# Performance work log

Measured on AMD Instinct MI355X. Metric: run time of the kernel, lower is better.

The kernel has to match this reference:

```python
import jax, jax.numpy as jnp
import numpy as np

B, NQ, NP, C, H = 8, 1024, 2048, 1024, 16
D = C // H  # head_dim = 64


def setup_inputs() -> dict:
    key = jax.random.key(0)
    ks = jax.random.split(key, 12)
    s = 1.0 / np.sqrt(C)
    inp = {
        "x": jax.random.normal(ks[0], (B, NQ, C), dtype=jnp.float32),
        "ctx": jax.random.normal(ks[1], (B, NP, C), dtype=jnp.float32),
        "freqs_cis": jax.random.normal(ks[2], (NP, D // 2, 2), dtype=jnp.float32),
        "wq": jax.random.normal(ks[3], (C, C), dtype=jnp.float32) * s,
        "bq": jnp.zeros((C,), dtype=jnp.float32),
        "wk": jax.random.normal(ks[4], (C, C), dtype=jnp.float32) * s,
        "bk": jnp.zeros((C,), dtype=jnp.float32),
        "wv": jax.random.normal(ks[5], (C, C), dtype=jnp.float32) * s,
        "bv": jnp.zeros((C,), dtype=jnp.float32),
        "wo": jax.random.normal(ks[6], (C, C), dtype=jnp.float32) * s,
        "bo": jnp.zeros((C,), dtype=jnp.float32),
    }
    return inp


def _apply_rope(k, freqs_cis):
    # k: [B, Np, H, D]; freqs_cis: [Np, D//2, 2] (cos, sin)
    b, n, h, d = k.shape
    kp = k.reshape(b, n, h, d // 2, 2)  # adjacent-pair complex convention
    kr, ki = kp[..., 0], kp[..., 1]
    cos = freqs_cis[None, :, None, :, 0]
    sin = freqs_cis[None, :, None, :, 1]
    out_r = kr * cos - ki * sin
    out_i = kr * sin + ki * cos
    return jnp.stack([out_r, out_i], axis=-1).reshape(b, n, h, d)


def reference(x, ctx, freqs_cis, wq, bq, wk, bk, wv, bv, wo, bo):
    b, nq, c = x.shape
    npx = ctx.shape[1]
    q = (jnp.einsum('bsc,oc->bso', x, wq) + bq).reshape(b, nq, H, D)
    k = (jnp.einsum('bsc,oc->bso', ctx, wk) + bk).reshape(b, npx, H, D)
    v = (jnp.einsum('bsc,oc->bso', ctx, wv) + bv).reshape(b, npx, H, D)
    k = _apply_rope(k, freqs_cis)
    scale = 1.0 / jnp.sqrt(jnp.asarray(D, dtype=q.dtype))
    scores = jnp.einsum('bqhd,bkhd->bhqk', q, k) * scale
    attn = jax.nn.softmax(scores, axis=-1)
    out = jnp.einsum('bhqk,bkhd->bqhd', attn, v).reshape(b, nq, c)
    return jnp.einsum('bsc,oc->bso', out, wo) + bo
```

## Files before the change

### kernel.cpp

```cpp
#include <hip/hip_runtime.h>
#include <stdint.h>

typedef __bf16 bf16;
typedef bf16 bf16x8 __attribute__((ext_vector_type(8)));
typedef float f32x4 __attribute__((ext_vector_type(4)));
typedef float f32x16 __attribute__((ext_vector_type(16)));
typedef uint32_t u32x4 __attribute__((ext_vector_type(4)));

static __device__ __forceinline__ void async_cp16(const bf16* gsrc, bf16* ldst) {
  __builtin_amdgcn_global_load_lds(
      (const __attribute__((address_space(1))) uint32_t*)gsrc,
      (__attribute__((address_space(3))) uint32_t*)ldst, 16, 0, 0);
}

static __device__ __forceinline__ f32x16 mfma32(bf16x8 a, bf16x8 b, f32x16 c) {
  return __builtin_amdgcn_mfma_f32_32x32x16_bf16(a, b, c, 0, 0, 0);
}

static __device__ __forceinline__ uint32_t cvtpk(float lo, float hi) {
  uint32_t r;
  asm("v_cvt_pk_bf16_f32 %0, %1, %2" : "=v"(r) : "v"(lo), "v"(hi));
  return r;
}
static __device__ __forceinline__ void plswap(uint32_t& a, uint32_t& b) {
  asm("v_permlane32_swap_b32 %0, %1" : "+v"(a), "+v"(b));
}

__global__ __launch_bounds__(256) void convert_all(
    const float* __restrict__ x, const float* __restrict__ ctx,
    const float* __restrict__ wq, const float* __restrict__ wk,
    const float* __restrict__ wv, const float* __restrict__ wo,
    bf16* __restrict__ xb, bf16* __restrict__ cb,
    bf16* __restrict__ wqb, bf16* __restrict__ wkb,
    bf16* __restrict__ wvb, bf16* __restrict__ wob) {
  int id = blockIdx.x;
  const float* s; bf16* d; int base;
  if (id < 8192)        { s = x;   d = xb;  base = id; }
  else if (id < 24576)  { s = ctx; d = cb;  base = id - 8192; }
  else if (id < 25600)  { s = wq;  d = wqb; base = id - 24576; }
  else if (id < 26624)  { s = wk;  d = wkb; base = id - 25600; }
  else if (id < 27648)  { s = wv;  d = wvb; base = id - 26624; }
  else                  { s = wo;  d = wob; base = id - 27648; }
  int i = base * 256 + threadIdx.x;
  float4 v = ((const float4*)s)[i];
  ushort4 o;
  o.x = __builtin_bit_cast(unsigned short, (bf16)v.x);
  o.y = __builtin_bit_cast(unsigned short, (bf16)v.y);
  o.z = __builtin_bit_cast(unsigned short, (bf16)v.z);
  o.w = __builtin_bit_cast(unsigned short, (bf16)v.w);
  ((ushort4*)d)[i] = o;
}

template <int OUT_F32, int BIAS_ROW = 0, int ROPE = 0>
__global__ __launch_bounds__(256) void gemm_bt(
    const bf16* __restrict__ A, const bf16* __restrict__ Bw,
    const float* __restrict__ bias, void* __restrict__ Cout,
    int M, int N, int K, float oscale, const float* __restrict__ freqs) {
  __shared__ __align__(16) bf16 sA[128 * 32];
  __shared__ __align__(16) bf16 sB[128 * 32];

  int per = gridDim.x >> 3;
  int id = blockIdx.x;
  int swz = (id & 7) * per + (id >> 3);
  int NB = N >> 7;
  int mb = swz / NB, nb = swz % NB;

  int t = threadIdx.x;
  int l = t & 63, w = t >> 6;
  int wr = (w >> 1) * 64, wc = (w & 1) * 64;
  int lr = l & 15, lk = (l >> 4) * 8;

  const bf16* Abase = A + (size_t)(mb * 128 + (t >> 2)) * K + (t & 3) * 8;
  const bf16* Bbase = Bw + (size_t)(nb * 128 + (t >> 2)) * K + (t & 3) * 8;
  bf16* ldsA = sA + w * 512;
  bf16* ldsB = sB + w * 512;

  f32x4 acc[4][4];
  for (int i = 0; i < 4; i++)
    for (int j = 0; j < 4; j++) acc[i][j] = f32x4{0.f, 0.f, 0.f, 0.f};

  for (int k0 = 0; k0 < K; k0 += 32) {
    async_cp16(Abase + k0, ldsA);
    async_cp16(Abase + k0 + (size_t)64 * K, ldsA + 2048);
    async_cp16(Bbase + k0, ldsB);
    async_cp16(Bbase + k0 + (size_t)64 * K, ldsB + 2048);
    __syncthreads();
    bf16x8 af[4], bfr[4];
    for (int mf = 0; mf < 4; mf++)
      af[mf] = *(const bf16x8*)&sA[(wr + mf * 16 + lr) * 32 + lk];
    for (int nf = 0; nf < 4; nf++)
      bfr[nf] = *(const bf16x8*)&sB[(wc + nf * 16 + lr) * 32 + lk];
    for (int mf = 0; mf < 4; mf++)
      for (int nf = 0; nf < 4; nf++)
        acc[mf][nf] = __builtin_amdgcn_mfma_f32_16x16x32_bf16(
            af[mf], bfr[nf], acc[mf][nf], 0, 0, 0);
    __syncthreads();
  }

  int row0 = mb * 128 + wr + (l >> 4) * 4;
  int col0 = nb * 128 + wc + lr;
  float sgn = (lr & 1) ? 1.f : -1.f;
  for (int nf = 0; nf < 4; nf++) {
    int c = col0 + nf * 16;
    float bi = BIAS_ROW ? 0.f : bias[c];
    for (int mf = 0; mf < 4; mf++)
      for (int j = 0; j < 4; j++) {
        int r = row0 + mf * 16 + j;
        float v = acc[mf][nf][j] + (BIAS_ROW ? bias[r] : bi);
        if (ROPE) {
          float pv = __shfl_xor(v, 1, 64);
          float2 f = ((const float2*)freqs)[(size_t)(r & 2047) * 32 + ((c & 63) >> 1)];
          v = v * f.x + sgn * pv * f.y;
        }
        v *= oscale;
        if (OUT_F32)
          ((float*)Cout)[(size_t)r * N + c] = v;
        else
          ((bf16*)Cout)[(size_t)r * N + c] = (bf16)v;
      }
  }
}

__global__ __launch_bounds__(256, 4) void attn_fwd(
    const bf16* __restrict__ Q, const bf16* __restrict__ Kb,
    const bf16* __restrict__ VT, bf16* __restrict__ O) {
  __shared__ __align__(16) bf16 sK[2][4096];
  __shared__ __align__(16) bf16 sV[2][4096];

  int nblk = blockIdx.x;
  int bh = (nblk & 7) * 16 + (nblk >> 6);
  int qt = (nblk >> 3) & 7;
  int b = bh >> 4, h = bh & 15;

  int t = threadIdx.x, l = t & 63, w = t >> 6;
  int ln = l & 31, hi = l >> 5;

  int qg = qt * 128 + w * 32 + ln;
  const bf16* qp = Q + ((size_t)(b * 1024 + qg) * 16 + h) * 64 + hi * 8;
  bf16x8 qf[4];
#pragma unroll
  for (int ds = 0; ds < 4; ds++) qf[ds] = *(const bf16x8*)(qp + ds * 16);

  const bf16* kbase = Kb + ((size_t)b * 2048 * 16 + h) * 64;
  const bf16* vtbase = VT + (size_t)(h * 64) * 16384 + b * 2048;

  int krow = w * 8 + (l >> 3);
  int cg1 = ((l & 7) ^ (krow & 7) ^ ((krow >> 3) & 7)) * 8;
  int r2 = krow + 32;
  int cg2 = ((l & 7) ^ (r2 & 7) ^ ((r2 >> 3) & 7)) * 8;

  auto stageK = [&](int kv0, int nb) {
    async_cp16(kbase + (size_t)(kv0 + krow) * 1024 + cg1, &sK[nb][w * 512]);
    async_cp16(kbase + (size_t)(kv0 + r2) * 1024 + cg2, &sK[nb][2048 + w * 512]);
  };
  auto stageV = [&](int kv0, int nb) {
    async_cp16(vtbase + (size_t)krow * 16384 + kv0 + cg1, &sV[nb][w * 512]);
    async_cp16(vtbase + (size_t)r2 * 16384 + kv0 + cg2, &sV[nb][2048 + w * 512]);
  };

  f32x16 o0, o1, s0, s1, lacc, zero16;
#pragma unroll
  for (int i = 0; i < 16; i++) {
    o0[i] = 0.f; o1[i] = 0.f; lacc[i] = 0.f; zero16[i] = 0.f;
  }
  uint32_t one2 = 0x3f803f80u;
  u32x4 onesw; onesw[0] = one2; onesw[1] = one2; onesw[2] = one2; onesw[3] = one2;
  bf16x8 onesf = __builtin_bit_cast(bf16x8, onesw);

  stageK(0, 0);
  stageV(0, 0);
  __syncthreads();
  int cur = 0;

  int x0 = ((ln & 7) ^ (ln >> 3)) << 3;
  int x1 = x0 ^ (4 << 3);

  for (int tt = 0; tt < 32; tt++) {
    if (tt < 31) { stageK(tt * 64 + 64, cur ^ 1); stageV(tt * 64 + 64, cur ^ 1); }

    __builtin_amdgcn_s_setprio(1);
    {
      int boff = hi * 8;
      bf16x8 kf0 = *(const bf16x8*)&sK[cur][ln * 64 + (boff ^ x0)];
      bf16x8 kf1 = *(const bf16x8*)&sK[cur][(ln + 32) * 64 + (boff ^ x1)];
      s0 = mfma32(kf0, qf[0], zero16);
      s1 = mfma32(kf1, qf[0], zero16);
    }
#pragma unroll
    for (int ds = 1; ds < 4; ds++) {
      int boff = ds * 16 + hi * 8;
      bf16x8 kf0 = *(const bf16x8*)&sK[cur][ln * 64 + (boff ^ x0)];
      bf16x8 kf1 = *(const bf16x8*)&sK[cur][(ln + 32) * 64 + (boff ^ x1)];
      s0 = mfma32(kf0, qf[ds], s0);
      s1 = mfma32(kf1, qf[ds], s1);
    }
    __builtin_amdgcn_s_setprio(0);

#pragma unroll
    for (int i = 0; i < 16; i++) {
      s0[i] = __builtin_amdgcn_exp2f(s0[i]);
      s1[i] = __builtin_amdgcn_exp2f(s1[i]);
    }

    bf16x8 pa[4];
    auto mkfrags = [&](const f32x16& sv, int base) {
#pragma unroll
      for (int u = 0; u < 2; u++) {
        uint32_t w0a = cvtpk(sv[8 * u + 0], sv[8 * u + 1]);
        uint32_t w0b = cvtpk(sv[8 * u + 4], sv[8 * u + 5]);
        plswap(w0a, w0b);
        uint32_t w1a = cvtpk(sv[8 * u + 2], sv[8 * u + 3]);
        uint32_t w1b = cvtpk(sv[8 * u + 6], sv[8 * u + 7]);
        plswap(w1a, w1b);
        u32x4 tmp;
        tmp[0] = w0a; tmp[1] = w1a; tmp[2] = w0b; tmp[3] = w1b;
        pa[base + u] = __builtin_bit_cast(bf16x8, tmp);
      }
    };
    mkfrags(s0, 0);
    mkfrags(s1, 2);

    __builtin_amdgcn_s_setprio(1);
#pragma unroll
    for (int ks = 0; ks < 4; ks++) {
      int koff = ks * 16 + hi * 8;
      bf16x8 vf0 = *(const bf16x8*)&sV[cur][ln * 64 + (koff ^ x0)];
      bf16x8 vf1 = *(const bf16x8*)&sV[cur][(ln + 32) * 64 + (koff ^ x1)];
      o0 = mfma32(vf0, pa[ks], o0);
      o1 = mfma32(vf1, pa[ks], o1);
      lacc = mfma32(onesf, pa[ks], lacc);
    }
    __builtin_amdgcn_s_setprio(0);

    __syncthreads();
    cur ^= 1;
  }

  float inv = __builtin_amdgcn_rcpf(lacc[0]);
  bf16* obase = O + ((size_t)(b * 1024 + qt * 128 + w * 32 + ln) * 16 + h) * 64;
#pragma unroll
  for (int g = 0; g < 4; g++) {
    ushort4 p0, p1;
    p0.x = __builtin_bit_cast(unsigned short, (bf16)(o0[4 * g + 0] * inv));
    p0.y = __builtin_bit_cast(unsigned short, (bf16)(o0[4 * g + 1] * inv));
    p0.z = __builtin_bit_cast(unsigned short, (bf16)(o0[4 * g + 2] * inv));
    p0.w = __builtin_bit_cast(unsigned short, (bf16)(o0[4 * g + 3] * inv));
    p1.x = __builtin_bit_cast(unsigned short, (bf16)(o1[4 * g + 0] * inv));
    p1.y = __builtin_bit_cast(unsigned short, (bf16)(o1[4 * g + 1] * inv));
    p1.z = __builtin_bit_cast(unsigned short, (bf16)(o1[4 * g + 2] * inv));
    p1.w = __builtin_bit_cast(unsigned short, (bf16)(o1[4 * g + 3] * inv));
    *(ushort4*)&obase[8 * g + 4 * hi] = p0;
    *(ushort4*)&obase[32 + 8 * g + 4 * hi] = p1;
  }
}

extern "C" void kernel_launch(void* const* d_in, const int* in_sizes, int n_in,
                              void* d_out, int out_size, void* d_ws, size_t ws_size,
                              hipStream_t stream) {
  const float* x     = (const float*)d_in[0];
  const float* ctx   = (const float*)d_in[1];
  const float* freqs = (const float*)d_in[2];
  const float* wq    = (const float*)d_in[3];
  const float* bq    = (const float*)d_in[4];
  const float* wk    = (const float*)d_in[5];
  const float* bk    = (const float*)d_in[6];
  const float* wv    = (const float*)d_in[7];
  const float* bv    = (const float*)d_in[8];
  const float* wo    = (const float*)d_in[9];
  const float* bo    = (const float*)d_in[10];

  char* p = (char*)d_ws;
  bf16* xb  = (bf16*)p; p += (size_t)8192 * 1024 * 2;
  bf16* cb  = (bf16*)p; p += (size_t)16384 * 1024 * 2;
  bf16* wqb = (bf16*)p; p += (size_t)1024 * 1024 * 2;
  bf16* wkb = (bf16*)p; p += (size_t)1024 * 1024 * 2;
  bf16* wvb = (bf16*)p; p += (size_t)1024 * 1024 * 2;
  bf16* wob = (bf16*)p; p += (size_t)1024 * 1024 * 2;
  bf16* qb  = (bf16*)p; p += (size_t)8192 * 1024 * 2;
  bf16* kb  = (bf16*)p; p += (size_t)16384 * 1024 * 2;
  bf16* vt  = (bf16*)p; p += (size_t)16384 * 1024 * 2;
  bf16* ob  = xb;

  const float K2 = 0.18033688011112042f;

  convert_all<<<28672, 256, 0, stream>>>(x, ctx, wq, wk, wv, wo,
                                         xb, cb, wqb, wkb, wvb, wob);
  gemm_bt<0><<<512, 256, 0, stream>>>(xb, wqb, bq, qb, 8192, 1024, 1024, K2, nullptr);
  gemm_bt<0, 0, 1><<<1024, 256, 0, stream>>>(cb, wkb, bk, kb, 16384, 1024, 1024, 1.0f, freqs);
  gemm_bt<0, 1><<<1024, 256, 0, stream>>>(wvb, cb, bv, vt, 1024, 16384, 1024, 1.0f, nullptr);
  attn_fwd<<<1024, 256, 0, stream>>>(qb, kb, vt, ob);
  gemm_bt<1><<<512, 256, 0, stream>>>(ob, wob, bo, d_out, 8192, 1024, 1024, 1.0f, nullptr);
}
```

Before: 297.2 us.

## Use 256x256 double-buffered pipelined GEMM for K and V projections

Adds a new 512-thread GEMM kernel with 256x256 output tiles, K-step 64, XOR-swizzled LDS layout, and double-buffered async global-to-LDS loads interleaved with MFMA phases under s_setprio. The K (with RoPE) and V-transpose projections switch to it, meant to raise arithmetic intensity and overlap memory with compute compared to the 128x128 single-buffered kernel. It uses 128KB of LDS per block, which may limit occupancy, and the grid shrinks to 256 blocks, which may underfill the GPU.

```diff
diff --git a/kernel.cpp b/kernel.cpp
--- a/kernel.cpp
+++ b/kernel.cpp
@@ -15,6 +15,9 @@
 
 static __device__ __forceinline__ f32x16 mfma32(bf16x8 a, bf16x8 b, f32x16 c) {
   return __builtin_amdgcn_mfma_f32_32x32x16_bf16(a, b, c, 0, 0, 0);
+}
+static __device__ __forceinline__ f32x4 mfma16(bf16x8 a, bf16x8 b, f32x4 c) {
+  return __builtin_amdgcn_mfma_f32_16x16x32_bf16(a, b, c, 0, 0, 0);
 }
 
 static __device__ __forceinline__ uint32_t cvtpk(float lo, float hi) {
@@ -92,8 +95,7 @@
       bfr[nf] = *(const bf16x8*)&sB[(wc + nf * 16 + lr) * 32 + lk];
     for (int mf = 0; mf < 4; mf++)
       for (int nf = 0; nf < 4; nf++)
-        acc[mf][nf] = __builtin_amdgcn_mfma_f32_16x16x32_bf16(
-            af[mf], bfr[nf], acc[mf][nf], 0, 0, 0);
+        acc[mf][nf] = mfma16(af[mf], bfr[nf], acc[mf][nf]);
     __syncthreads();
   }
 
@@ -121,6 +123,169 @@
   }
 }
 
+template <int OUT_F32, int BIAS_ROW, int ROPE>
+__global__ __launch_bounds__(512, 2) void gemm256(
+    const bf16* __restrict__ A, const bf16* __restrict__ Bw,
+    const float* __restrict__ bias, void* __restrict__ Cout,
+    int N, int K, float oscale, const float* __restrict__ freqs) {
+  __shared__ __align__(16) bf16 sA[2][16384];
+  __shared__ __align__(16) bf16 sB[2][16384];
+
+  int per = gridDim.x >> 3;
+  int id = blockIdx.x;
+  int swz = (id & 7) * per + (id >> 3);
+  int NB = N >> 8;
+  int mb = swz / NB, nb = swz % NB;
+
+  int tid = threadIdx.x;
+  int l = tid & 63, w = tid >> 6;
+  int wm = w >> 2, wn = w & 3;
+  int lr = l & 15, kg = l >> 4;
+
+  int rw = w * 8 + (l >> 3);
+  int cs = ((l & 7) ^ ((l >> 3) & 7)) * 8;
+  const bf16* Ab = A + (size_t)(mb * 256 + rw) * K + cs;
+  const bf16* Bb = Bw + (size_t)(nb * 256 + rw) * K + cs;
+
+  auto stA = [&](int kt, int half, int buf) {
+    const bf16* g = Ab + (size_t)(half * 128) * K + kt * 64;
+    bf16* d = &sA[buf][half * 8192 + w * 512];
+    async_cp16(g, d);
+    async_cp16(g + (size_t)64 * K, d + 4096);
+  };
+  auto stB = [&](int kt, int half, int buf) {
+    const bf16* g = Bb + (size_t)(half * 128) * K + kt * 64;
+    bf16* d = &sB[buf][half * 8192 + w * 512];
+    async_cp16(g, d);
+    async_cp16(g + (size_t)64 * K, d + 4096);
+  };
+
+  f32x4 acc[8][4];
+#pragma unroll
+  for (int i = 0; i < 8; i++)
+#pragma unroll
+    for (int j = 0; j < 4; j++) acc[i][j] = f32x4{0.f, 0.f, 0.f, 0.f};
+
+  int NT = K >> 6;
+
+  stA(0, 0, 0); stA(0, 1, 0); stB(0, 0, 0); stB(0, 1, 0);
+  asm volatile("s_waitcnt vmcnt(0)" ::: "memory");
+  __builtin_amdgcn_s_barrier();
+
+  int cur = 0;
+  for (int t = 0; t < NT; ++t) {
+    bool pf = (t + 1 < NT);
+    if (pf) {
+      stA(t + 1, 0, cur ^ 1);
+      asm volatile("s_waitcnt vmcnt(2)" ::: "memory");
+    } else {
+      asm volatile("s_waitcnt vmcnt(0)" ::: "memory");
+    }
+    __builtin_amdgcn_s_barrier();
+
+    const bf16* pA = sA[cur];
+    const bf16* pB = sB[cur];
+    bf16x8 afr[4][2], bq0[2][2], bq1[2][2];
+
+    auto rdA = [&](int mh, int mf, int ks) {
+      int rT = wm * 128 + mh * 64 + mf * 16 + lr;
+      return *(const bf16x8*)&pA[rT * 64 + (((ks << 2) | kg) ^ (lr & 7)) * 8];
+    };
+    auto rdB = [&](int nfg, int ks) {
+      int rT = wn * 64 + nfg * 16 + lr;
+      return *(const bf16x8*)&pB[rT * 64 + (((ks << 2) | kg) ^ (lr & 7)) * 8];
+    };
+
+#pragma unroll
+    for (int mf = 0; mf < 4; mf++) { afr[mf][0] = rdA(0, mf, 0); afr[mf][1] = rdA(0, mf, 1); }
+#pragma unroll
+    for (int nf = 0; nf < 2; nf++) { bq0[nf][0] = rdB(nf, 0); bq0[nf][1] = rdB(nf, 1); }
+    __builtin_amdgcn_s_barrier();
+    __builtin_amdgcn_s_setprio(1);
+#pragma unroll
+    for (int mf = 0; mf < 4; mf++)
+#pragma unroll
+      for (int nf = 0; nf < 2; nf++)
+#pragma unroll
+        for (int ks = 0; ks < 2; ks++)
+          acc[mf][nf] = mfma16(afr[mf][ks], bq0[nf][ks], acc[mf][nf]);
+    __builtin_amdgcn_s_setprio(0);
+    __builtin_amdgcn_s_barrier();
+
+#pragma unroll
+    for (int nf = 0; nf < 2; nf++) { bq1[nf][0] = rdB(2 + nf, 0); bq1[nf][1] = rdB(2 + nf, 1); }
+    if (pf) stA(t + 1, 1, cur ^ 1);
+    __builtin_amdgcn_s_barrier();
+    __builtin_amdgcn_s_setprio(1);
+#pragma unroll
+    for (int mf = 0; mf < 4; mf++)
+#pragma unroll
+      for (int nf = 0; nf < 2; nf++)
+#pragma unroll
+        for (int ks = 0; ks < 2; ks++)
+          acc[mf][2 + nf] = mfma16(afr[mf][ks], bq1[nf][ks], acc[mf][2 + nf]);
+    __builtin_amdgcn_s_setprio(0);
+    __builtin_amdgcn_s_barrier();
+
+#pragma unroll
+    for (int mf = 0; mf < 4; mf++) { afr[mf][0] = rdA(1, mf, 0); afr[mf][1] = rdA(1, mf, 1); }
+    if (pf) stB(t + 1, 0, cur ^ 1);
+    __builtin_amdgcn_s_barrier();
+    __builtin_amdgcn_s_setprio(1);
+#pragma unroll
+    for (int mf = 0; mf < 4; mf++)
+#pragma unroll
+      for (int nf = 0; nf < 2; nf++)
+#pragma unroll
+        for (int ks = 0; ks < 2; ks++)
+          acc[4 + mf][2 + nf] = mfma16(afr[mf][ks], bq1[nf][ks], acc[4 + mf][2 + nf]);
+    __builtin_amdgcn_s_setprio(0);
+    __builtin_amdgcn_s_barrier();
+
+    if (pf) stB(t + 1, 1, cur ^ 1);
+    __builtin_amdgcn_s_barrier();
+    __builtin_amdgcn_s_setprio(1);
+#pragma unroll
+    for (int mf = 0; mf < 4; mf++)
+#pragma unroll
+      for (int nf = 0; nf < 2; nf++)
+#pragma unroll
+        for (int ks = 0; ks < 2; ks++)
+          acc[4 + mf][nf] = mfma16(afr[mf][ks], bq0[nf][ks], acc[4 + mf][nf]);
+    __builtin_amdgcn_s_setprio(0);
+    __builtin_amdgcn_s_barrier();
+
+    cur ^= 1;
+  }
+
+  int row0 = mb * 256 + wm * 128 + (l >> 4) * 4;
+  int col0 = nb * 256 + wn * 64 + lr;
+  float sgn = (lr & 1) ? 1.f : -1.f;
+#pragma unroll
+  for (int fc = 0; fc < 4; fc++) {
+    int c = col0 + fc * 16;
+    float bi = BIAS_ROW ? 0.f : bias[c];
+#pragma unroll
+    for (int fr = 0; fr < 8; fr++) {
+#pragma unroll
+      for (int j = 0; j < 4; j++) {
+        int r = row0 + fr * 16 + j;
+        float v = acc[fr][fc][j] + (BIAS_ROW ? bias[r] : bi);
+        if (ROPE) {
+          float pv = __shfl_xor(v, 1, 64);
+          float2 f = ((const float2*)freqs)[(size_t)(r & 2047) * 32 + ((c & 63) >> 1)];
+          v = v * f.x + sgn * pv * f.y;
+        }
+        v *= oscale;
+        if (OUT_F32)
+          ((float*)Cout)[(size_t)r * N + c] = v;
+        else
+          ((bf16*)Cout)[(size_t)r * N + c] = (bf16)v;
+      }
+    }
+  }
+}
+
 __global__ __launch_bounds__(256, 4) void attn_fwd(
     const bf16* __restrict__ Q, const bf16* __restrict__ Kb,
     const bf16* __restrict__ VT, bf16* __restrict__ O) {
@@ -286,8 +451,8 @@
   convert_all<<<28672, 256, 0, stream>>>(x, ctx, wq, wk, wv, wo,
                                          xb, cb, wqb, wkb, wvb, wob);
   gemm_bt<0><<<512, 256, 0, stream>>>(xb, wqb, bq, qb, 8192, 1024, 1024, K2, nullptr);
-  gemm_bt<0, 0, 1><<<1024, 256, 0, stream>>>(cb, wkb, bk, kb, 16384, 1024, 1024, 1.0f, freqs);
-  gemm_bt<0, 1><<<1024, 256, 0, stream>>>(wvb, cb, bv, vt, 1024, 16384, 1024, 1.0f, nullptr);
+  gemm256<0, 0, 1><<<256, 512, 0, stream>>>(cb, wkb, bk, kb, 1024, 1024, 1.0f, freqs);
+  gemm256<0, 1, 0><<<256, 512, 0, stream>>>(wvb, cb, bv, vt, 16384, 1024, 1.0f, nullptr);
   attn_fwd<<<1024, 256, 0, stream>>>(qb, kb, vt, ob);
   gemm_bt<1><<<512, 256, 0, stream>>>(ob, wob, bo, d_out, 8192, 1024, 1024, 1.0f, nullptr);
 }
```

Result: faster. 277.1 us (median of 3 runs) (-6.8%).

## Replace 128x128 GEMM with 256x256-tile, 4-stage pipelined, LDS-swizzled GEMM

Applied to the files above, without the earlier changes.

Replaces the projection GEMM kernel with a 512-thread kernel that computes 256x256 output tiles, so each block reuses more data per load. Global-to-LDS async copies run through a 4-buffer pipeline with vmcnt-based waits and a single barrier per k-step, so loads overlap the MFMA work. It also XOR-swizzles the LDS layout to avoid bank conflicts and raises wave priority around the MFMAs. K is hardcoded to 1024. The Q and output GEMMs now launch only 128 blocks, which may leave CUs idle.

```diff
diff --git a/kernel.cpp b/kernel.cpp
--- a/kernel.cpp
+++ b/kernel.cpp
@@ -15,6 +15,9 @@
 
 static __device__ __forceinline__ f32x16 mfma32(bf16x8 a, bf16x8 b, f32x16 c) {
   return __builtin_amdgcn_mfma_f32_32x32x16_bf16(a, b, c, 0, 0, 0);
+}
+static __device__ __forceinline__ f32x4 mfma16(bf16x8 a, bf16x8 b, f32x4 c) {
+  return __builtin_amdgcn_mfma_f32_16x16x32_bf16(a, b, c, 0, 0, 0);
 }
 
 static __device__ __forceinline__ uint32_t cvtpk(float lo, float hi) {
@@ -51,62 +54,105 @@
   ((ushort4*)d)[i] = o;
 }
 
-template <int OUT_F32, int BIAS_ROW = 0, int ROPE = 0>
-__global__ __launch_bounds__(256) void gemm_bt(
+template <int OUT_F32, int BIAS_ROW, int ROPE>
+__global__ __launch_bounds__(512, 2) void gemm256(
     const bf16* __restrict__ A, const bf16* __restrict__ Bw,
     const float* __restrict__ bias, void* __restrict__ Cout,
-    int M, int N, int K, float oscale, const float* __restrict__ freqs) {
-  __shared__ __align__(16) bf16 sA[128 * 32];
-  __shared__ __align__(16) bf16 sB[128 * 32];
+    int N, float oscale, const float* __restrict__ freqs) {
+  __shared__ __align__(16) bf16 sA[4][8192];
+  __shared__ __align__(16) bf16 sB[4][8192];
+  const int K = 1024;
 
   int per = gridDim.x >> 3;
   int id = blockIdx.x;
   int swz = (id & 7) * per + (id >> 3);
-  int NB = N >> 7;
+  int NB = N >> 8;
   int mb = swz / NB, nb = swz % NB;
 
-  int t = threadIdx.x;
-  int l = t & 63, w = t >> 6;
-  int wr = (w >> 1) * 64, wc = (w & 1) * 64;
-  int lr = l & 15, lk = (l >> 4) * 8;
-
-  const bf16* Abase = A + (size_t)(mb * 128 + (t >> 2)) * K + (t & 3) * 8;
-  const bf16* Bbase = Bw + (size_t)(nb * 128 + (t >> 2)) * K + (t & 3) * 8;
-  bf16* ldsA = sA + w * 512;
-  bf16* ldsB = sB + w * 512;
-
-  f32x4 acc[4][4];
-  for (int i = 0; i < 4; i++)
+  int tid = threadIdx.x;
+  int l = tid & 63, w = tid >> 6;
+  int wm = w >> 2, wn = w & 3;
+  int lr = l & 15, kg = l >> 4;
+
+  int rw = w * 16 + (l >> 2);
+  int cs = ((l & 3) ^ ((l >> 3) & 3)) * 8;
+  const bf16* Ab = A + (size_t)(mb * 256 + rw) * K + cs;
+  const bf16* Bb = Bw + (size_t)(nb * 256 + rw) * K + cs;
+
+  auto stage = [&](int kt) {
+    int buf = kt & 3;
+    async_cp16(Ab + kt * 32, &sA[buf][w * 512]);
+    async_cp16(Ab + kt * 32 + (size_t)128 * K, &sA[buf][w * 512 + 4096]);
+    async_cp16(Bb + kt * 32, &sB[buf][w * 512]);
+    async_cp16(Bb + kt * 32 + (size_t)128 * K, &sB[buf][w * 512 + 4096]);
+  };
+
+  f32x4 acc[8][4];
+#pragma unroll
+  for (int i = 0; i < 8; i++)
+#pragma unroll
     for (int j = 0; j < 4; j++) acc[i][j] = f32x4{0.f, 0.f, 0.f, 0.f};
 
-  for (int k0 = 0; k0 < K; k0 += 32) {
-    async_cp16(Abase + k0, ldsA);
-    async_cp16(Abase + k0 + (size_t)64 * K, ldsA + 2048);
-    async_cp16(Bbase + k0, ldsB);
-    async_cp16(Bbase + k0 + (size_t)64 * K, ldsB + 2048);
-    __syncthreads();
-    bf16x8 af[4], bfr[4];
-    for (int mf = 0; mf < 4; mf++)
-      af[mf] = *(const bf16x8*)&sA[(wr + mf * 16 + lr) * 32 + lk];
-    for (int nf = 0; nf < 4; nf++)
-      bfr[nf] = *(const bf16x8*)&sB[(wc + nf * 16 + lr) * 32 + lk];
-    for (int mf = 0; mf < 4; mf++)
+  int xr = (kg ^ ((lr >> 1) & 3)) * 8;
+
+  auto compute = [&](int t) {
+    const bf16* pA = sA[t & 3];
+    const bf16* pB = sB[t & 3];
+    bf16x8 af[8], bfv[4];
+#pragma unroll
+    for (int mf = 0; mf < 8; mf++) {
+      int ar = wm * 128 + mf * 16 + lr;
+      af[mf] = *(const bf16x8*)&pA[ar * 32 + xr];
+    }
+#pragma unroll
+    for (int nf = 0; nf < 4; nf++) {
+      int br = wn * 64 + nf * 16 + lr;
+      bfv[nf] = *(const bf16x8*)&pB[br * 32 + xr];
+    }
+    __builtin_amdgcn_s_setprio(1);
+#pragma unroll
+    for (int mf = 0; mf < 8; mf++)
+#pragma unroll
       for (int nf = 0; nf < 4; nf++)
-        acc[mf][nf] = __builtin_amdgcn_mfma_f32_16x16x32_bf16(
-            af[mf], bfr[nf], acc[mf][nf], 0, 0, 0);
-    __syncthreads();
-  }
-
-  int row0 = mb * 128 + wr + (l >> 4) * 4;
-  int col0 = nb * 128 + wc + lr;
+        acc[mf][nf] = mfma16(af[mf], bfv[nf], acc[mf][nf]);
+    __builtin_amdgcn_s_setprio(0);
+  };
+
+  stage(0); stage(1); stage(2);
+  asm volatile("s_waitcnt vmcnt(8)" ::: "memory");
+  __builtin_amdgcn_s_barrier();
+  __builtin_amdgcn_sched_barrier(0);
+
+  for (int t = 0; t < 29; ++t) {
+    stage(t + 3);
+    compute(t);
+    asm volatile("s_waitcnt vmcnt(8)" ::: "memory");
+    __builtin_amdgcn_s_barrier();
+    __builtin_amdgcn_sched_barrier(0);
+  }
+  compute(29);
+  asm volatile("s_waitcnt vmcnt(4)" ::: "memory");
+  __builtin_amdgcn_s_barrier();
+  __builtin_amdgcn_sched_barrier(0);
+  compute(30);
+  asm volatile("s_waitcnt vmcnt(0)" ::: "memory");
+  __builtin_amdgcn_s_barrier();
+  __builtin_amdgcn_sched_barrier(0);
+  compute(31);
+
+  int row0 = mb * 256 + wm * 128 + (l >> 4) * 4;
+  int col0 = nb * 256 + wn * 64 + lr;
   float sgn = (lr & 1) ? 1.f : -1.f;
-  for (int nf = 0; nf < 4; nf++) {
-    int c = col0 + nf * 16;
+#pragma unroll
+  for (int fc = 0; fc < 4; fc++) {
+    int c = col0 + fc * 16;
     float bi = BIAS_ROW ? 0.f : bias[c];
-    for (int mf = 0; mf < 4; mf++)
+#pragma unroll
+    for (int fr = 0; fr < 8; fr++) {
+#pragma unroll
       for (int j = 0; j < 4; j++) {
-        int r = row0 + mf * 16 + j;
-        float v = acc[mf][nf][j] + (BIAS_ROW ? bias[r] : bi);
+        int r = row0 + fr * 16 + j;
+        float v = acc[fr][fc][j] + (BIAS_ROW ? bias[r] : bi);
         if (ROPE) {
           float pv = __shfl_xor(v, 1, 64);
           float2 f = ((const float2*)freqs)[(size_t)(r & 2047) * 32 + ((c & 63) >> 1)];
@@ -118,6 +164,7 @@
         else
           ((bf16*)Cout)[(size_t)r * N + c] = (bf16)v;
       }
+    }
   }
 }
 
@@ -285,9 +332,9 @@
 
   convert_all<<<28672, 256, 0, stream>>>(x, ctx, wq, wk, wv, wo,
                                          xb, cb, wqb, wkb, wvb, wob);
-  gemm_bt<0><<<512, 256, 0, stream>>>(xb, wqb, bq, qb, 8192, 1024, 1024, K2, nullptr);
-  gemm_bt<0, 0, 1><<<1024, 256, 0, stream>>>(cb, wkb, bk, kb, 16384, 1024, 1024, 1.0f, freqs);
-  gemm_bt<0, 1><<<1024, 256, 0, stream>>>(wvb, cb, bv, vt, 1024, 16384, 1024, 1.0f, nullptr);
+  gemm256<0, 0, 0><<<128, 512, 0, stream>>>(xb, wqb, bq, qb, 1024, K2, nullptr);
+  gemm256<0, 0, 1><<<256, 512, 0, stream>>>(cb, wkb, bk, kb, 1024, 1.0f, freqs);
+  gemm256<0, 1, 0><<<256, 512, 0, stream>>>(wvb, cb, bv, vt, 16384, 1.0f, nullptr);
   attn_fwd<<<1024, 256, 0, stream>>>(qb, kb, vt, ob);
-  gemm_bt<1><<<512, 256, 0, stream>>>(ob, wob, bo, d_out, 8192, 1024, 1024, 1.0f, nullptr);
-}
+  gemm256<1, 0, 0><<<128, 512, 0, stream>>>(ob, wob, bo, d_out, 1024, 1.0f, nullptr);
+}
```

Result: slower. 305.3 us (+2.7%).
